# Kernel optimization log

Measured on AMD Instinct MI355X. Metric: run time of the kernel, lower is better.

The kernel has to match this reference:

```python
import jax, jax.numpy as jnp
from jax import lax
import numpy as np

KERNEL_SIZE = 24

def setup_inputs() -> dict:
    key = jax.random.key(0)
    k1, k2, k3, k4 = jax.random.split(key, 4)
    B, C, T = 16, 1024, 3000
    x = jax.random.normal(k1, (B, C, T, 1), dtype=jnp.float32)
    alpha = jax.random.uniform(k2, (C,), dtype=jnp.float32)   # in (0,1): decaying kernels
    beta = jax.random.normal(k3, (C,), dtype=jnp.float32)
    theta = jax.random.uniform(k4, (C,), dtype=jnp.float32)
    return {"x": x, "alpha": alpha, "beta": beta, "theta": theta}

def _cos_approx(x):
    x2 = x * x
    return 1.0 - 0.5 * x2 + (x2 * x2) * (1.0 / 24.0)

def reference(x, alpha, beta, theta):
    B, C, T, _ = x.shape
    K = KERNEL_SIZE
    t_idx = jnp.arange(K, dtype=x.dtype)                      # (K,)
    log_alpha = jnp.log(jnp.clip(alpha, 1e-6))                # (C,)
    decay = jnp.exp(log_alpha[:, None] * t_idx)               # (C,K)
    phase = _cos_approx(theta[:, None] * t_idx)               # (C,K)
    kernel = (beta[:, None] * decay * phase)[:, None, :]      # (C,1,K) depthwise
    # causal depthwise conv1d: left-pad K-1 (torch F.conv1d and lax conv are both correlations)
    y = lax.conv_general_dilated(
        x[..., 0], kernel,
        window_strides=(1,), padding=[(K - 1, 0)],
        dimension_numbers=("NCH", "OIH", "NCH"),
        feature_group_count=C,
    )                                                         # (B,C,T)
    return y[..., None]                                       # (B,C,T,1)
```

## Files before the change

### kernel.cpp

```cpp
#include <hip/hip_runtime.h>


#define KSZ   24
#define TILE  1024
#define BLOCK 256
#define T_LEN 3000
#define C_CH  1024
#define B_N   16

__device__ __forceinline__ float cos_approx(float v) {
    float v2 = v * v;
    return 1.0f - 0.5f * v2 + (v2 * v2) * (1.0f / 24.0f);
}

__global__ __launch_bounds__(BLOCK) void ssm4d_conv(
        const float* __restrict__ x,
        const float* __restrict__ alpha,
        const float* __restrict__ beta,
        const float* __restrict__ theta,
        float* __restrict__ y) {
    __shared__ __align__(16) float s[KSZ + TILE];
    __shared__ float sw[KSZ];

    const int tile = blockIdx.x;
    const int row  = blockIdx.y;
    const int c    = row & (C_CH - 1);
    const long base = (long)row * T_LEN;
    const int t0  = tile * TILE;
    const int tid = threadIdx.x;

    if (tid < KSZ) {
        const int k = (KSZ - 1) - tid;
        const float a  = fmaxf(alpha[c], 1e-6f);
        const float la = logf(a);
        const float dec = expf(la * (float)k);
        const float ph  = cos_approx(theta[c] * (float)k);
        sw[tid] = beta[c] * dec * ph;

        const int th = t0 - KSZ + tid;
        s[tid] = (th >= 0) ? x[base + th] : 0.0f;
    }

    const int t = t0 + 4 * tid;
    if (t < T_LEN) {
        *(float4*)(s + KSZ + 4 * tid) = *(const float4*)(x + base + t);
    }
    __syncthreads();
    if (t >= T_LEN) return;

    float arr[28];
#pragma unroll
    for (int q = 0; q < 7; ++q) {
        float4 v = *(const float4*)(s + 4 * tid + 4 * q);
        arr[4 * q + 0] = v.x; arr[4 * q + 1] = v.y;
        arr[4 * q + 2] = v.z; arr[4 * q + 3] = v.w;
    }
    float wr[KSZ];
#pragma unroll
    for (int d = 0; d < KSZ; ++d) wr[d] = sw[d];

    float a0 = 0.f, a1 = 0.f, a2 = 0.f, a3 = 0.f;
#pragma unroll
    for (int d = 0; d < KSZ; ++d) {
        a0 = fmaf(wr[d], arr[24 + 0 - d], a0);
        a1 = fmaf(wr[d], arr[24 + 1 - d], a1);
        a2 = fmaf(wr[d], arr[24 + 2 - d], a2);
        a3 = fmaf(wr[d], arr[24 + 3 - d], a3);
    }
    *(float4*)(y + base + t) = make_float4(a0, a1, a2, a3);
}

extern "C" void kernel_launch(void* const* d_in, const int* in_sizes, int n_in,
                              void* d_out, int out_size, void* d_ws, size_t ws_size,
                              hipStream_t stream) {
    const float* x     = (const float*)d_in[0];
    const float* alpha = (const float*)d_in[1];
    const float* beta  = (const float*)d_in[2];
    const float* theta = (const float*)d_in[3];
    float* y = (float*)d_out;

    dim3 grid((T_LEN + TILE - 1) / TILE, B_N * C_CH);
    ssm4d_conv<<<grid, BLOCK, 0, stream>>>(x, alpha, beta, theta, y);
}
```

Baseline: 345.6 us.

## Precompute weights in a separate kernel and load halos directly from global memory

Moves the per-channel filter weight computation into a small prologue kernel that writes to workspace. The conv kernel drops shared memory and __syncthreads, and each thread reads its 32-element window (24 halo + 8 outputs) straight from global via float4 loads. Each thread now computes 8 outputs instead of 4, using 128-thread blocks. The aim is to remove per-block transcendental math and the LDS staging barrier, at the cost of redundant overlapping global reads of halos (mostly L1/L2 hits) and an extra kernel launch.

New measurement: 336.5 us. 2.6% less time.

```diff
diff --git a/kernel.cpp b/kernel.cpp
--- a/kernel.cpp
+++ b/kernel.cpp
@@ -2,72 +2,81 @@
 
 
 #define KSZ   24
-#define TILE  1024
-#define BLOCK 256
 #define T_LEN 3000
 #define C_CH  1024
 #define B_N   16
+#define OPT   8
+#define TPB   128
+#define TILE  (TPB * OPT)
 
 __device__ __forceinline__ float cos_approx(float v) {
     float v2 = v * v;
     return 1.0f - 0.5f * v2 + (v2 * v2) * (1.0f / 24.0f);
 }
 
-__global__ __launch_bounds__(BLOCK) void ssm4d_conv(
+__global__ void ssm4d_weights(const float* __restrict__ alpha,
+                              const float* __restrict__ beta,
+                              const float* __restrict__ theta,
+                              float* __restrict__ w) {
+    const int i = blockIdx.x * blockDim.x + threadIdx.x;
+    if (i >= C_CH * KSZ) return;
+    const int c = i / KSZ;
+    const int d = i - c * KSZ;
+    const int k = (KSZ - 1) - d;
+    const float a   = fmaxf(alpha[c], 1e-6f);
+    const float dec = expf(logf(a) * (float)k);
+    w[i] = beta[c] * dec * cos_approx(theta[c] * (float)k);
+}
+
+__global__ __launch_bounds__(TPB) void ssm4d_conv(
         const float* __restrict__ x,
-        const float* __restrict__ alpha,
-        const float* __restrict__ beta,
-        const float* __restrict__ theta,
+        const float* __restrict__ w,
         float* __restrict__ y) {
-    __shared__ __align__(16) float s[KSZ + TILE];
-    __shared__ float sw[KSZ];
-
-    const int tile = blockIdx.x;
     const int row  = blockIdx.y;
     const int c    = row & (C_CH - 1);
     const long base = (long)row * T_LEN;
-    const int t0  = tile * TILE;
-    const int tid = threadIdx.x;
+    const int t    = blockIdx.x * TILE + threadIdx.x * OPT;
+    if (t >= T_LEN) return;
 
-    if (tid < KSZ) {
-        const int k = (KSZ - 1) - tid;
-        const float a  = fmaxf(alpha[c], 1e-6f);
-        const float la = logf(a);
-        const float dec = expf(la * (float)k);
-        const float ph  = cos_approx(theta[c] * (float)k);
-        sw[tid] = beta[c] * dec * ph;
-
-        const int th = t0 - KSZ + tid;
-        s[tid] = (th >= 0) ? x[base + th] : 0.0f;
+    float wr[KSZ];
+    const float4* wp = (const float4*)(w + c * KSZ);
+#pragma unroll
+    for (int q = 0; q < KSZ / 4; ++q) {
+        float4 v = wp[q];
+        wr[4 * q + 0] = v.x; wr[4 * q + 1] = v.y;
+        wr[4 * q + 2] = v.z; wr[4 * q + 3] = v.w;
     }
 
-    const int t = t0 + 4 * tid;
-    if (t < T_LEN) {
-        *(float4*)(s + KSZ + 4 * tid) = *(const float4*)(x + base + t);
+    float arr[KSZ + OPT];
+    if (t >= KSZ) {
+        const float4* xp = (const float4*)(x + base + t - KSZ);
+#pragma unroll
+        for (int q = 0; q < (KSZ + OPT) / 4; ++q) {
+            float4 v = xp[q];
+            arr[4 * q + 0] = v.x; arr[4 * q + 1] = v.y;
+            arr[4 * q + 2] = v.z; arr[4 * q + 3] = v.w;
+        }
+    } else {
+#pragma unroll
+        for (int p = 0; p < KSZ + OPT; ++p) {
+            const int idx = t - KSZ + p;
+            arr[p] = (idx >= 0) ? x[base + idx] : 0.0f;
+        }
     }
-    __syncthreads();
-    if (t >= T_LEN) return;
 
-    float arr[28];
+    float acc[OPT];
 #pragma unroll
-    for (int q = 0; q < 7; ++q) {
-        float4 v = *(const float4*)(s + 4 * tid + 4 * q);
-        arr[4 * q + 0] = v.x; arr[4 * q + 1] = v.y;
-        arr[4 * q + 2] = v.z; arr[4 * q + 3] = v.w;
-    }
-    float wr[KSZ];
-#pragma unroll
-    for (int d = 0; d < KSZ; ++d) wr[d] = sw[d];
-
-    float a0 = 0.f, a1 = 0.f, a2 = 0.f, a3 = 0.f;
+    for (int m = 0; m < OPT; ++m) acc[m] = 0.0f;
 #pragma unroll
     for (int d = 0; d < KSZ; ++d) {
-        a0 = fmaf(wr[d], arr[24 + 0 - d], a0);
-        a1 = fmaf(wr[d], arr[24 + 1 - d], a1);
-        a2 = fmaf(wr[d], arr[24 + 2 - d], a2);
-        a3 = fmaf(wr[d], arr[24 + 3 - d], a3);
+#pragma unroll
+        for (int m = 0; m < OPT; ++m)
+            acc[m] = fmaf(wr[d], arr[KSZ + m - d], acc[m]);
     }
-    *(float4*)(y + base + t) = make_float4(a0, a1, a2, a3);
+
+    float4* yp = (float4*)(y + base + t);
+    yp[0] = make_float4(acc[0], acc[1], acc[2], acc[3]);
+    yp[1] = make_float4(acc[4], acc[5], acc[6], acc[7]);
 }
 
 extern "C" void kernel_launch(void* const* d_in, const int* in_sizes, int n_in,
@@ -78,7 +87,10 @@
     const float* beta  = (const float*)d_in[2];
     const float* theta = (const float*)d_in[3];
     float* y = (float*)d_out;
+    float* w = (float*)d_ws;
+
+    ssm4d_weights<<<(C_CH * KSZ + 255) / 256, 256, 0, stream>>>(alpha, beta, theta, w);
 
     dim3 grid((T_LEN + TILE - 1) / TILE, B_N * C_CH);
-    ssm4d_conv<<<grid, BLOCK, 0, stream>>>(x, alpha, beta, theta, y);
+    ssm4d_conv<<<grid, TPB, 0, stream>>>(x, w, y);
 }
```
